# Performance work log

Measured on AMD Instinct MI355X. Metric: run time of the kernel, lower is better.

The kernel has to match this reference:

```python
import jax, jax.numpy as jnp
import numpy as np
import math

B, L, H, D = 4, 2048, 8, 64
FACTOR = 5
SAMPLE_K = min(FACTOR * math.ceil(math.log(L)), L)   # u = 40
N_TOP = min(FACTOR * math.ceil(math.log(L)), L)      # U_part = 40


def setup_inputs() -> dict:
    key = jax.random.key(0)
    k1, k2, k3, k4 = jax.random.split(key, 4)
    return {
        "queries": jax.random.normal(k1, (B, L, H, D), dtype=jnp.float32),
        "keys": jax.random.normal(k2, (B, L, H, D), dtype=jnp.float32),
        "values": jax.random.normal(k3, (B, L, H, D), dtype=jnp.float32),
        "index_sample": jax.random.randint(k4, (L, SAMPLE_K), 0, L, dtype=jnp.int32),
    }


def reference(queries, keys, values, index_sample):
    # queries/keys/values: [B, L, H, D] -> [B, H, L, D]
    Q = jnp.transpose(queries, (0, 2, 1, 3))
    K = jnp.transpose(keys, (0, 2, 1, 3))
    V = jnp.transpose(values, (0, 2, 1, 3))
    Bc, Hc, L_Q, Dc = Q.shape
    L_K = K.shape[2]
    scale = 1.0 / math.sqrt(Dc)

    # --- _prob_QK: random K sampling, sparsity measure M, top-n_top queries ---
    K_samp = K[:, :, index_sample, :]                       # [B,H,L_Q,S,D]
    QK_samp = jnp.einsum('bhqd,bhqsd->bhqs', Q, K_samp)     # [B,H,L_Q,S]
    M = QK_samp.max(axis=-1) - QK_samp.sum(axis=-1) / L_K   # [B,H,L_Q]
    _, M_top = jax.lax.top_k(M, N_TOP)                      # [B,H,n_top]
    Q_reduce = jnp.take_along_axis(Q, M_top[..., None], axis=2)  # [B,H,n_top,D]
    scores = jnp.einsum('bhud,bhkd->bhuk', Q_reduce, K) * scale  # [B,H,n_top,L_K]

    # --- initial context (mask_flag=False): mean of V broadcast over queries ---
    context = jnp.broadcast_to(V.mean(axis=2, keepdims=True), (Bc, Hc, L_Q, Dc))

    # --- update context at selected query positions ---
    attn = jax.nn.softmax(scores, axis=-1)                  # [B,H,n_top,L_K]
    upd = jnp.einsum('bhuk,bhkd->bhud', attn, V)            # [B,H,n_top,D]
    bi = jnp.arange(Bc)[:, None, None]
    hi = jnp.arange(Hc)[None, :, None]
    context = context.at[bi, hi, M_top].set(upd)

    return jnp.transpose(context, (0, 2, 1, 3))             # [B,L_Q,H,D]
```

## Files before the change

### kernel.cpp

```cpp
#include <hip/hip_runtime.h>
#include <math.h>

#define B_ 4
#define L_ 2048
#define H_ 8
#define D_ 64
#define SK 40
#define NTOP 40
#define HD (H_*D_)

typedef float4 f4;

static __device__ __forceinline__ float rl(float v, int l) {
  return __int_as_float(__builtin_amdgcn_readlane(__float_as_int(v), l));
}

static __device__ __forceinline__ int xcd_swz(int bid, int cpx) {
  return (bid & 7) * cpx + (bid >> 3);
}

__global__ __launch_bounds__(256) void k_sampleM(
    const float* __restrict__ Q, const float* __restrict__ K,
    const int* __restrict__ samp, float* __restrict__ M)
{
  int bid = xcd_swz(blockIdx.x, 256);
  int w = threadIdx.x >> 6, lane = threadIdx.x & 63;
  int g = lane >> 3, li = lane & 7;
  int gq = (bid * 4 + w) * 8 + g;
  int qpos = gq & (L_ - 1);
  int bh = gq >> 11;
  int h = bh & (H_ - 1), b = bh >> 3;
  const size_t bhoff = (size_t)b * L_ * HD + (size_t)h * D_;
  const f4* qrow = (const f4*)(Q + bhoff + (size_t)qpos * HD);
  f4 q0 = qrow[li], q1 = qrow[li + 8];
  const int* srow = samp + qpos * SK;
  const float* kb = K + bhoff;
  float mx = -INFINITY, sm = 0.f;
  #pragma unroll 4
  for (int s = 0; s < SK; ++s) {
    int ki = srow[s];
    const f4* krow = (const f4*)(kb + (size_t)ki * HD);
    f4 k0 = krow[li], k1 = krow[li + 8];
    float p = q0.x*k0.x + q0.y*k0.y + q0.z*k0.z + q0.w*k0.w
            + q1.x*k1.x + q1.y*k1.y + q1.z*k1.z + q1.w*k1.w;
    p += __shfl_xor(p, 1);
    p += __shfl_xor(p, 2);
    p += __shfl_xor(p, 4);
    mx = fmaxf(mx, p);
    sm += p;
  }
  if (li == 0) M[gq] = mx - sm * (1.0f / L_);
}

__global__ __launch_bounds__(256) void k_topk(
    const float* __restrict__ M, int* __restrict__ top)
{
  __shared__ unsigned hist[256];
  __shared__ unsigned sfx[256];
  __shared__ int s_sel, s_k;
  __shared__ unsigned s_ngt, s_neq;
  __shared__ int eqidx[L_];
  int bh = blockIdx.x, t = threadIdx.x;

  unsigned v[8];
  #pragma unroll
  for (int j = 0; j < 8; ++j) {
    unsigned u = __float_as_uint(M[bh * L_ + t + j * 256]);
    v[j] = (u & 0x80000000u) ? ~u : (u | 0x80000000u);
  }

  unsigned prefix = 0;
  int kneed = NTOP;
  for (int shift = 24; shift >= 0; shift -= 8) {
    hist[t] = 0;
    __syncthreads();
    unsigned msk = (shift == 24) ? 0u : (0xFFFFFFFFu << (shift + 8));
    #pragma unroll
    for (int j = 0; j < 8; ++j)
      if ((v[j] & msk) == prefix)
        atomicAdd(&hist[(v[j] >> shift) & 255u], 1u);
    __syncthreads();
    sfx[t] = hist[t];
    __syncthreads();
    #pragma unroll
    for (int off = 1; off < 256; off <<= 1) {
      unsigned add = (t + off < 256) ? sfx[t + off] : 0u;
      __syncthreads();
      sfx[t] += add;
      __syncthreads();
    }
    unsigned Sm = sfx[t];
    unsigned Sn = (t < 255) ? sfx[t + 1] : 0u;
    if (Sm >= (unsigned)kneed && Sn < (unsigned)kneed) {
      s_sel = t;
      s_k = kneed - (int)Sn;
    }
    __syncthreads();
    prefix |= ((unsigned)s_sel) << shift;
    kneed = s_k;
  }
  if (t == 0) { s_ngt = 0; s_neq = 0; }
  __syncthreads();
  #pragma unroll
  for (int j = 0; j < 8; ++j) {
    if (v[j] > prefix) {
      unsigned p = atomicAdd(&s_ngt, 1u);
      top[bh * NTOP + p] = t + j * 256;
    } else if (v[j] == prefix) {
      unsigned p = atomicAdd(&s_neq, 1u);
      eqidx[p] = t + j * 256;
    }
  }
  __syncthreads();
  if (t == 0) {
    int base = NTOP - kneed;
    int n = (int)s_neq;
    for (int r = 0; r < kneed; ++r) {
      int bm = 0x7fffffff, bp = 0;
      for (int i = 0; i < n; ++i)
        if (eqidx[i] < bm) { bm = eqidx[i]; bp = i; }
      top[bh * NTOP + base + r] = bm;
      eqidx[bp] = 0x7fffffff;
    }
  }
}

__global__ __launch_bounds__(256) void k_vmean1(
    const float* __restrict__ V, float* __restrict__ part)
{
  __shared__ f4 red[16][16];
  int bh = blockIdx.x >> 5, chunk = blockIdx.x & 31;
  int h = bh & 7, b = bh >> 3;
  int t = threadIdx.x;
  int d4 = t & 15, rg = t >> 4;
  const f4* vb = (const f4*)(V + (size_t)b * L_ * HD + (size_t)h * D_);
  f4 s = {0.f, 0.f, 0.f, 0.f};
  int row0 = chunk * 64 + rg;
  #pragma unroll
  for (int r = 0; r < 4; ++r) {
    f4 v = vb[(size_t)(row0 + r * 16) * (HD / 4) + d4];
    s.x += v.x; s.y += v.y; s.z += v.z; s.w += v.w;
  }
  red[rg][d4] = s;
  __syncthreads();
  #pragma unroll
  for (int off = 8; off; off >>= 1) {
    if (rg < off) {
      f4 a = red[rg][d4], bb = red[rg + off][d4];
      a.x += bb.x; a.y += bb.y; a.z += bb.z; a.w += bb.w;
      red[rg][d4] = a;
    }
    __syncthreads();
  }
  if (rg == 0) ((f4*)part)[(size_t)blockIdx.x * 16 + d4] = red[0][d4];
}

__global__ __launch_bounds__(64) void k_vmean2(
    const float* __restrict__ part, float* __restrict__ vm)
{
  int bh = blockIdx.x, lane = threadIdx.x;
  float s = 0.f;
  #pragma unroll 8
  for (int c = 0; c < 32; ++c)
    s += part[(size_t)(bh * 32 + c) * 64 + lane];
  vm[bh * 64 + lane] = s * (1.0f / L_);
}

__global__ __launch_bounds__(256) void k_fill(
    const float* __restrict__ vm, float* __restrict__ out)
{
  int i = blockIdx.x * 256 + threadIdx.x;
  int d4 = i & 15;
  int h  = (i >> 4) & 7;
  int b  = i >> 18;
  ((f4*)out)[i] = ((const f4*)vm)[(b * 8 + h) * 16 + d4];
}

__global__ __launch_bounds__(256, 4) void k_attn(
    const float* __restrict__ Q, const float* __restrict__ K,
    const float* __restrict__ V, const int* __restrict__ top,
    float* __restrict__ pm, float* __restrict__ pl, float* __restrict__ pacc)
{
  __shared__ float plds[4][5][64];
  int bid = xcd_swz(blockIdx.x, 256);
  int lane = threadIdx.x & 63;
  int w = __builtin_amdgcn_readfirstlane(threadIdx.x >> 6);
  int gw = bid * 4 + w;
  int uq = gw & 7;
  int ch = (gw >> 3) & 31;
  int bh = gw >> 8;
  int h = bh & 7, b = bh >> 3;
  const size_t bhoff = (size_t)b * L_ * HD + (size_t)h * D_;
  const int kbase = ch * 64;

  f4 kr[16];
  {
    const f4* krow = (const f4*)(K + bhoff + (size_t)(kbase + lane) * HD);
    #pragma unroll
    for (int j = 0; j < 16; ++j) kr[j] = krow[j];
  }
  const float* qr[5];
  #pragma unroll
  for (int u = 0; u < 5; ++u) {
    int pos = __builtin_amdgcn_readfirstlane(top[bh * NTOP + uq * 5 + u]);
    qr[u] = Q + bhoff + (size_t)pos * HD;
  }
  float s[5] = {0.f, 0.f, 0.f, 0.f, 0.f};
  #pragma unroll
  for (int j = 0; j < 16; ++j) {
    f4 kv = kr[j];
    #pragma unroll
    for (int u = 0; u < 5; ++u) {
      s[u] = fmaf(qr[u][4*j+0], kv.x, s[u]);
      s[u] = fmaf(qr[u][4*j+1], kv.y, s[u]);
      s[u] = fmaf(qr[u][4*j+2], kv.z, s[u]);
      s[u] = fmaf(qr[u][4*j+3], kv.w, s[u]);
    }
  }
  #pragma unroll
  for (int u = 0; u < 5; ++u) {
    float sv = s[u] * 0.125f;
    float mx = sv;
    #pragma unroll
    for (int off = 32; off; off >>= 1) mx = fmaxf(mx, __shfl_xor(mx, off));
    float pv = __expf(sv - mx);
    float ls = pv;
    #pragma unroll
    for (int off = 32; off; off >>= 1) ls += __shfl_xor(ls, off);
    plds[w][u][lane] = pv;
    int e = (bh * 32 + ch) * NTOP + uq * 5 + u;
    if (lane == 0) { pm[e] = mx; pl[e] = ls; }
  }
  int kg = lane >> 4, dq = lane & 15;
  f4 acc4[5];
  #pragma unroll
  for (int u = 0; u < 5; ++u) acc4[u] = f4{0.f, 0.f, 0.f, 0.f};
  const f4* vrow = (const f4*)(V + bhoff) + (size_t)(kbase + kg) * (HD/4) + dq;
  #pragma unroll
  for (int j = 0; j < 16; ++j) {
    f4 vv = vrow[(size_t)(4*j) * (HD/4)];
    int kk = 4*j + kg;
    #pragma unroll
    for (int u = 0; u < 5; ++u) {
      float pj = plds[w][u][kk];
      acc4[u].x = fmaf(pj, vv.x, acc4[u].x);
      acc4[u].y = fmaf(pj, vv.y, acc4[u].y);
      acc4[u].z = fmaf(pj, vv.z, acc4[u].z);
      acc4[u].w = fmaf(pj, vv.w, acc4[u].w);
    }
  }
  #pragma unroll
  for (int u = 0; u < 5; ++u) {
    acc4[u].x += __shfl_xor(acc4[u].x, 16);
    acc4[u].y += __shfl_xor(acc4[u].y, 16);
    acc4[u].z += __shfl_xor(acc4[u].z, 16);
    acc4[u].w += __shfl_xor(acc4[u].w, 16);
    acc4[u].x += __shfl_xor(acc4[u].x, 32);
    acc4[u].y += __shfl_xor(acc4[u].y, 32);
    acc4[u].z += __shfl_xor(acc4[u].z, 32);
    acc4[u].w += __shfl_xor(acc4[u].w, 32);
  }
  if (kg == 0) {
    #pragma unroll
    for (int u = 0; u < 5; ++u) {
      size_t e = (size_t)(bh * 32 + ch) * NTOP + uq * 5 + u;
      ((f4*)(pacc + e * 64))[dq] = acc4[u];
    }
  }
}

__global__ __launch_bounds__(256) void k_merge(
    const float* __restrict__ pm, const float* __restrict__ pl,
    const float* __restrict__ pacc, const int* __restrict__ top,
    float* __restrict__ out)
{
  int w = threadIdx.x >> 6, lane = threadIdx.x & 63;
  int gw = blockIdx.x * 4 + w;
  int bh = gw / NTOP, u = gw - bh * NTOP;
  int h = bh & 7, b = bh >> 3;
  int c = lane & 31;
  int e = (bh * 32 + c) * NTOP + u;
  float mc = pm[e], lc = pl[e];
  if (lane >= 32) { mc = -INFINITY; lc = 0.f; }
  float Mg = mc;
  #pragma unroll
  for (int off = 32; off; off >>= 1) Mg = fmaxf(Mg, __shfl_xor(Mg, off));
  float fc = __expf(mc - Mg);
  float fl = fc * lc;
  float Lg = fl;
  #pragma unroll
  for (int off = 32; off; off >>= 1) Lg += __shfl_xor(Lg, off);
  float o = 0.f;
  const float* pa = pacc + ((size_t)(bh * 32) * NTOP + u) * 64 + lane;
  #pragma unroll
  for (int cc = 0; cc < 32; ++cc)
    o = fmaf(rl(fc, cc), pa[(size_t)cc * NTOP * 64], o);
  int pos = top[bh * NTOP + u];
  out[((size_t)(b * L_ + pos) * H_ + h) * D_ + lane] = o / Lg;
}

extern "C" void kernel_launch(void* const* d_in, const int* in_sizes, int n_in,
                              void* d_out, int out_size, void* d_ws, size_t ws_size,
                              hipStream_t stream) {
  const float* Q = (const float*)d_in[0];
  const float* K = (const float*)d_in[1];
  const float* V = (const float*)d_in[2];
  const int* samp = (const int*)d_in[3];
  float* out = (float*)d_out;

  float* ws    = (float*)d_ws;
  float* M     = ws;
  float* vmean = M + 65536;
  float* pm    = vmean + 2048;
  float* pl    = pm + 40960;
  float* pacc  = pl + 40960;
  int*   top   = (int*)(pacc + 2621440);
  float* vpart = pacc;

  hipLaunchKernelGGL(k_sampleM, dim3(2048), dim3(256), 0, stream, Q, K, samp, M);
  hipLaunchKernelGGL(k_topk,   dim3(32),   dim3(256), 0, stream, M, top);
  hipLaunchKernelGGL(k_vmean1, dim3(1024), dim3(256), 0, stream, V, vpart);
  hipLaunchKernelGGL(k_vmean2, dim3(32),   dim3(64),  0, stream, vpart, vmean);
  hipLaunchKernelGGL(k_fill,   dim3(4096), dim3(256), 0, stream, vmean, out);
  hipLaunchKernelGGL(k_attn,   dim3(2048), dim3(256), 0, stream, Q, K, V, top, pm, pl, pacc);
  hipLaunchKernelGGL(k_merge,  dim3(320),  dim3(256), 0, stream, pm, pl, pacc, top, out);
}
```

Measured before the change: 84.65 us.

## Compute attention scores with coalesced K rows and shuffle reductions

Reworks the QK score stage in k_attn. Each lane used to hold a full K row in 16 float4 registers and read Q values through uniform pointers. Now groups of 16 lanes read one K row as coalesced float4 pieces, multiply by a per-lane Q fragment, reduce with xor shuffles, and store the scores to LDS for the softmax step. This is meant to cut register pressure and make K loads coalesced, at the cost of more shuffles and LDS traffic. The occupancy hint in launch_bounds is also dropped.

```diff
diff --git a/kernel.cpp b/kernel.cpp
--- a/kernel.cpp
+++ b/kernel.cpp
@@ -176,7 +176,7 @@
   ((f4*)out)[i] = ((const f4*)vm)[(b * 8 + h) * 16 + d4];
 }
 
-__global__ __launch_bounds__(256, 4) void k_attn(
+__global__ __launch_bounds__(256) void k_attn(
     const float* __restrict__ Q, const float* __restrict__ K,
     const float* __restrict__ V, const int* __restrict__ top,
     float* __restrict__ pm, float* __restrict__ pl, float* __restrict__ pacc)
@@ -184,7 +184,7 @@
   __shared__ float plds[4][5][64];
   int bid = xcd_swz(blockIdx.x, 256);
   int lane = threadIdx.x & 63;
-  int w = __builtin_amdgcn_readfirstlane(threadIdx.x >> 6);
+  int w = threadIdx.x >> 6;
   int gw = bid * 4 + w;
   int uq = gw & 7;
   int ch = (gw >> 3) & 31;
@@ -192,34 +192,31 @@
   int h = bh & 7, b = bh >> 3;
   const size_t bhoff = (size_t)b * L_ * HD + (size_t)h * D_;
   const int kbase = ch * 64;
-
-  f4 kr[16];
-  {
-    const f4* krow = (const f4*)(K + bhoff + (size_t)(kbase + lane) * HD);
-    #pragma unroll
-    for (int j = 0; j < 16; ++j) kr[j] = krow[j];
-  }
-  const float* qr[5];
+  int kg = lane >> 4, dq = lane & 15;
+
+  f4 qf[5];
   #pragma unroll
   for (int u = 0; u < 5; ++u) {
-    int pos = __builtin_amdgcn_readfirstlane(top[bh * NTOP + uq * 5 + u]);
-    qr[u] = Q + bhoff + (size_t)pos * HD;
-  }
-  float s[5] = {0.f, 0.f, 0.f, 0.f, 0.f};
+    int pos = top[bh * NTOP + uq * 5 + u];
+    qf[u] = ((const f4*)(Q + bhoff + (size_t)pos * HD))[dq];
+  }
+  const f4* krow = (const f4*)(K + bhoff) + (size_t)(kbase + kg) * (HD/4) + dq;
   #pragma unroll
   for (int j = 0; j < 16; ++j) {
-    f4 kv = kr[j];
+    f4 kv = krow[(size_t)(4*j) * (HD/4)];
     #pragma unroll
     for (int u = 0; u < 5; ++u) {
-      s[u] = fmaf(qr[u][4*j+0], kv.x, s[u]);
-      s[u] = fmaf(qr[u][4*j+1], kv.y, s[u]);
-      s[u] = fmaf(qr[u][4*j+2], kv.z, s[u]);
-      s[u] = fmaf(qr[u][4*j+3], kv.w, s[u]);
+      float p = qf[u].x*kv.x + qf[u].y*kv.y + qf[u].z*kv.z + qf[u].w*kv.w;
+      p += __shfl_xor(p, 1);
+      p += __shfl_xor(p, 2);
+      p += __shfl_xor(p, 4);
+      p += __shfl_xor(p, 8);
+      if (dq == 0) plds[w][u][4*j + kg] = p;
     }
   }
   #pragma unroll
   for (int u = 0; u < 5; ++u) {
-    float sv = s[u] * 0.125f;
+    float sv = plds[w][u][lane] * 0.125f;
     float mx = sv;
     #pragma unroll
     for (int off = 32; off; off >>= 1) mx = fmaxf(mx, __shfl_xor(mx, off));
@@ -231,7 +228,6 @@
     int e = (bh * 32 + ch) * NTOP + uq * 5 + u;
     if (lane == 0) { pm[e] = mx; pl[e] = ls; }
   }
-  int kg = lane >> 4, dq = lane & 15;
   f4 acc4[5];
   #pragma unroll
   for (int u = 0; u < 5; ++u) acc4[u] = f4{0.f, 0.f, 0.f, 0.f};
```

Result: slower. 107.2 us (+26.6%).
